# Optimization experiments

Measured on AMD Instinct MI355X. Metric: run time of the kernel, lower is better.

The kernel has to match this reference:

```python
import jax, jax.numpy as jnp
import numpy as np

D_IN, N_LAT, B, H, W = 512, 16384, 16, 16, 16

def setup_inputs() -> dict:
    key = jax.random.key(0)
    k1, k2, k3, k4, k5 = jax.random.split(key, 5)
    x = jax.random.normal(k1, (B, D_IN, H, W), dtype=jnp.float32)
    enc_w = jax.random.normal(k2, (N_LAT, D_IN), dtype=jnp.float32) / np.sqrt(D_IN)
    enc_b = jax.random.normal(k3, (N_LAT,), dtype=jnp.float32) * 0.01
    dec_w = jax.random.normal(k4, (D_IN, N_LAT), dtype=jnp.float32)
    # normalize_decoder=True: unit-norm columns (per latent)
    dec_w = dec_w / (jnp.linalg.norm(dec_w, axis=0, keepdims=True) + 1e-7)
    dec_b = jax.random.normal(k5, (D_IN,), dtype=jnp.float32) * 0.01
    return {"x": x, "enc_w": enc_w, "enc_b": enc_b, "dec_w": dec_w, "dec_b": dec_b, "k": 32}

def reference(x, enc_w, enc_b, dec_w, dec_b, k):
    # encoder: 1x1 conv == pointwise channel matmul, then ReLU
    pre = jax.nn.relu(jnp.einsum('bchw,lc->bhwl', x, enc_w) + enc_b)  # [B,H,W,L]
    # top-k over latent dim (last axis)
    top_acts, top_idx = jax.lax.top_k(pre, k)  # [B,H,W,k]
    # sparse decode: scatter-into-dense + 1x1 conv == gather decoder columns
    # and weighted sum (topk indices are distinct, so scatter == this gather-sum)
    w_g = dec_w.T[top_idx]                      # [B,H,W,k,d_in]
    sae_out = jnp.einsum('bhwk,bhwkd->bdhw', top_acts, w_g) + dec_b[None, :, None, None]
    e = sae_out - x
    l2_loss = jnp.sum(e.astype(jnp.float32) ** 2)
    mu = x.mean(axis=(0, 2, 3)).reshape(1, -1, 1, 1)
    total_variance = jnp.sum(((x - mu).astype(jnp.float32)) ** 2)
    fvu = (l2_loss / total_variance).astype(e.dtype)
    # match torch layout: [B, k, H, W]
    top_acts_out = jnp.transpose(top_acts, (0, 3, 1, 2))
    top_idx_out = jnp.transpose(top_idx, (0, 3, 1, 2))
    auxk_loss = jnp.zeros((), dtype=sae_out.dtype)
    multi_topk_fvu = jnp.zeros((), dtype=sae_out.dtype)
    return sae_out, top_acts_out, top_idx_out, fvu, auxk_loss, multi_topk_fvu
```

## Files before the change

### kernel.cpp

```cpp
#include <hip/hip_runtime.h>
#include <stdint.h>

typedef __attribute__((ext_vector_type(4))) int i32x4;

#define TN 2.45f
#define PMARG 0.10f
#define CAP 224
#define SORT2 128

__device__ inline float bf2f(unsigned short u) { return __uint_as_float(((unsigned int)u) << 16); }
__device__ inline unsigned short f2bf(float f) {
    unsigned int x = __float_as_uint(f);
    return (unsigned short)((x + 0x7FFFu + ((x >> 16) & 1u)) >> 16);
}

template <typename T>
__device__ inline void gload16(const T* g, T* l) {
    __builtin_amdgcn_global_load_lds((const __attribute__((address_space(1))) void*)g,
                                     (__attribute__((address_space(3))) void*)l, 16, 0, 0);
}

__global__ __launch_bounds__(256) void t1_x(const float* __restrict__ x, float* __restrict__ xTf,
                                            float* __restrict__ thrS,
                                            double* __restrict__ S, double* __restrict__ Q) {
    __shared__ float tile[64][65];
    int b = blockIdx.z, c0 = blockIdx.x * 64, hw0 = blockIdx.y * 64;
    int tid = threadIdx.x, g = tid >> 6, ln = tid & 63;
    for (int i = 0; i < 16; i++) {
        int cl = g * 16 + i;
        tile[cl][ln] = x[(size_t)(b * 512 + c0 + cl) * 256 + hw0 + ln];
    }
    __syncthreads();
    float s1 = 0.0f, s2 = 0.0f;
    for (int i = 0; i < 16; i++) {
        int hl = g * 16 + i;
        float v = tile[ln][hl];
        xTf[(size_t)(b * 256 + hw0 + hl) * 512 + c0 + ln] = v;
        s1 += v;
        s2 += v * v;
        float s = v * v;
        for (int off = 32; off; off >>= 1) s += __shfl_down(s, off, 64);
        if (ln == 0) atomicAdd(&thrS[b * 256 + hw0 + hl], s);
    }
    atomicAdd(&S[c0 + ln], (double)s1);
    atomicAdd(&Q[c0 + ln], (double)s2);
}

__device__ inline void quant_row(const float* __restrict__ src, signed char* __restrict__ dst,
                                 float* __restrict__ scale, int row, int lane) {
    const float4* s4 = (const float4*)(src + (size_t)row * 512);
    float4 a = s4[lane * 2], b = s4[lane * 2 + 1];
    float m = fmaxf(fmaxf(fmaxf(fabsf(a.x), fabsf(a.y)), fmaxf(fabsf(a.z), fabsf(a.w))),
                    fmaxf(fmaxf(fabsf(b.x), fabsf(b.y)), fmaxf(fabsf(b.z), fabsf(b.w))));
    for (int off = 32; off; off >>= 1) m = fmaxf(m, __shfl_xor(m, off, 64));
    m = fmaxf(m, 1e-20f);
    float inv = 127.0f / m;
    int q0 = __float2int_rn(a.x * inv), q1 = __float2int_rn(a.y * inv);
    int q2 = __float2int_rn(a.z * inv), q3 = __float2int_rn(a.w * inv);
    int q4 = __float2int_rn(b.x * inv), q5 = __float2int_rn(b.y * inv);
    int q6 = __float2int_rn(b.z * inv), q7 = __float2int_rn(b.w * inv);
    unsigned int w0 = (q0 & 255) | ((q1 & 255) << 8) | ((q2 & 255) << 16) | ((unsigned)(q3 & 255) << 24);
    unsigned int w1 = (q4 & 255) | ((q5 & 255) << 8) | ((q6 & 255) << 16) | ((unsigned)(q7 & 255) << 24);
    *(uint2*)(dst + (size_t)row * 512 + lane * 8) = make_uint2(w0, w1);
    if (lane == 0) scale[row] = m * (1.0f / 127.0f);
}

__global__ __launch_bounds__(256) void k_quant(const float* __restrict__ xTf, signed char* __restrict__ xq,
                                               float* __restrict__ sx, const float* __restrict__ enc_w,
                                               signed char* __restrict__ wq, float* __restrict__ sw) {
    int r = blockIdx.x * 4 + (threadIdx.x >> 6), lane = threadIdx.x & 63;
    if (r < 4096) quant_row(xTf, xq, sx, r, lane);
    else quant_row(enc_w, wq, sw, r - 4096, lane);
}

__global__ __launch_bounds__(256) void t3_decw(const float* __restrict__ w, unsigned short* __restrict__ wT) {
    __shared__ float tile[64][65];
    int l0 = blockIdx.x * 64, d0 = blockIdx.y * 64;
    int tid = threadIdx.x, g = tid >> 6, ln = tid & 63;
    for (int i = 0; i < 16; i++) {
        int dl = g * 16 + i;
        tile[dl][ln] = w[(size_t)(d0 + dl) * 16384 + l0 + ln];
    }
    __syncthreads();
    for (int i = 0; i < 16; i++) {
        int ll = g * 16 + i;
        wT[(size_t)(l0 + ll) * 512 + d0 + ln] = f2bf(tile[ln][ll]);
    }
}

#define SBAR                                   \
    __builtin_amdgcn_sched_barrier(0);         \
    __builtin_amdgcn_s_barrier();              \
    __builtin_amdgcn_sched_barrier(0);
#define VMW4 { asm volatile("s_waitcnt vmcnt(4)" ::: "memory"); __builtin_amdgcn_sched_barrier(0); }
#define VMW0 { asm volatile("s_waitcnt vmcnt(0)" ::: "memory"); __builtin_amdgcn_sched_barrier(0); }

__global__ __launch_bounds__(256) void k_gemm(const signed char* __restrict__ xq,
                                              const signed char* __restrict__ wq,
                                              const float* __restrict__ sx, const float* __restrict__ sw,
                                              const float* __restrict__ thrS,
                                              int* __restrict__ cnt, unsigned int* __restrict__ cand) {
    __shared__ __align__(16) signed char As[3][128 * 64];
    __shared__ __align__(16) signed char Bs[3][128 * 64];
    int tid = threadIdx.x, wid = tid >> 6, lane = tid & 63;

    int lin = blockIdx.x + blockIdx.y * gridDim.x;
    int swz = (lin & 7) * 512 + (lin >> 3);
    int bx = swz >> 5;
    int by = swz & 31;
    int m0 = by * 128, n0 = bx * 128;
    int wr = wid >> 1, wc = wid & 1;

    i32x4 acc[4][4];
#pragma unroll
    for (int mi = 0; mi < 4; mi++)
#pragma unroll
        for (int ni = 0; ni < 4; ni++)
#pragma unroll
            for (int j = 0; j < 4; j++) acc[mi][ni][j] = 0;

    int srow = lane >> 2;

#define STAGE(bufi, kt)                                                                            \
    {                                                                                              \
        signed char* Ad = &As[bufi][0];                                                            \
        signed char* Bd = &Bs[bufi][0];                                                            \
        _Pragma("unroll")                                                                          \
        for (int i_ = 0; i_ < 2; i_++) {                                                           \
            int ch_ = wid * 2 + i_;                                                                \
            int row_ = ch_ * 16 + srow;                                                            \
            int sc_ = (((lane & 3) ^ ((row_ >> 1) & 3)) << 4);                                     \
            gload16(xq + (size_t)(m0 + row_) * 512 + (kt) + sc_, Ad + ch_ * 1024);                 \
            gload16(wq + (size_t)(n0 + row_) * 512 + (kt) + sc_, Bd + ch_ * 1024);                 \
        }                                                                                          \
    }

    STAGE(0, 0)
    STAGE(1, 64)
#pragma unroll
    for (int t = 0; t < 8; t++) {
        int cur = t % 3;
        if (t < 7) VMW4
        else VMW0
        SBAR
        if (t < 6) STAGE((t + 2) % 3, (t + 2) * 64)
        const signed char* Ac = &As[cur][0];
        const signed char* Bc = &Bs[cur][0];
        i32x4 a[4], b[4];
#pragma unroll
        for (int mi = 0; mi < 4; mi++) {
            int r = wr * 64 + mi * 16 + (lane & 15);
            int slot = (lane >> 4) ^ ((r >> 1) & 3);
            a[mi] = *(const i32x4*)&Ac[r * 64 + slot * 16];
        }
#pragma unroll
        for (int ni = 0; ni < 4; ni++) {
            int r = wc * 64 + ni * 16 + (lane & 15);
            int slot = (lane >> 4) ^ ((r >> 1) & 3);
            b[ni] = *(const i32x4*)&Bc[r * 64 + slot * 16];
        }
#pragma unroll
        for (int mi = 0; mi < 4; mi++)
#pragma unroll
            for (int ni = 0; ni < 4; ni++)
                acc[mi][ni] = __builtin_amdgcn_mfma_i32_16x16x64_i8(a[mi], b[ni], acc[mi][ni], 0, 0, 0);
    }
#undef STAGE

    float swl[4];
#pragma unroll
    for (int ni = 0; ni < 4; ni++) swl[ni] = sw[n0 + wc * 64 + ni * 16 + (lane & 15)];
#pragma unroll
    for (int mi = 0; mi < 4; mi++)
#pragma unroll
        for (int j = 0; j < 4; j++) {
            int pixel = m0 + wr * 64 + mi * 16 + (lane >> 4) * 4 + j;
            float tv = TN * sqrtf(thrS[pixel] * (1.0f / 512.0f));
            float sxp = sx[pixel];
#pragma unroll
            for (int ni = 0; ni < 4; ni++) {
                float v = (float)acc[mi][ni][j] * (sxp * swl[ni]);
                if (v >= tv) {
                    int lat = n0 + wc * 64 + ni * 16 + (lane & 15);
                    int slot = atomicAdd(&cnt[pixel], 1);
                    if (slot < CAP) cand[pixel * CAP + slot] = ((unsigned)f2bf(v) << 16) | (unsigned)lat;
                }
            }
        }
}

__global__ __launch_bounds__(256) void k_topk(const float* __restrict__ xTf, const float* __restrict__ enc_w,
                                              const float* __restrict__ enc_b, const int* __restrict__ cnt,
                                              const unsigned int* __restrict__ cand,
                                              const unsigned short* __restrict__ dwT,
                                              const float* __restrict__ dec_b,
                                              float* __restrict__ out_acts, float* __restrict__ out_idx,
                                              float* __restrict__ out_sae, double* __restrict__ l2acc) {
    __shared__ __align__(16) float xrow[512];
    __shared__ unsigned long long skey2[SORT2];
    __shared__ int npool;
    __shared__ float sa[32];
    __shared__ int si[32];
    __shared__ double red[256];
    int p = blockIdx.x, tid = threadIdx.x;
    for (int i = tid; i < 512; i += 256) xrow[i] = xTf[(size_t)p * 512 + i];
    if (tid < SORT2) skey2[tid] = ~0ull;
    if (tid == 0) npool = 0;
    int c = cnt[p];
    if (c > CAP) c = CAP;
    unsigned int pk = (tid < c) ? cand[p * CAP + tid] : 0u;
    unsigned int bfb = pk >> 16;
    int lo = 0, hi = 65535;
    for (int it = 0; it < 16; it++) {
        int mid = (lo + hi + 1) >> 1;
        int n = __syncthreads_count(tid < c && bfb >= (unsigned)mid);
        if (n >= 32) lo = mid; else hi = mid - 1;
    }
    float pthr = bf2f((unsigned short)lo) - PMARG;
    __syncthreads();
    if (tid < c && bf2f((unsigned short)bfb) >= pthr) {
        int slot = atomicAdd(&npool, 1);
        if (slot < SORT2) {
            int lat = (int)(pk & 16383u);
            const float4* w4 = (const float4*)(enc_w + (size_t)lat * 512);
            const float4* x4 = (const float4*)xrow;
            float acc = 0.0f;
            for (int q = 0; q < 128; q++) {
                float4 w = w4[q];
                float4 xv = x4[q];
                acc = __fmaf_rn(xv.x, w.x, acc);
                acc = __fmaf_rn(xv.y, w.y, acc);
                acc = __fmaf_rn(xv.z, w.z, acc);
                acc = __fmaf_rn(xv.w, w.w, acc);
            }
            float pre = __fadd_rn(acc, enc_b[lat]);
            unsigned long long key;
            if (pre > 0.0f) {
                key = ((unsigned long long)(0xFFFFFFFFu - __float_as_uint(pre)) << 32) | (unsigned)lat;
            } else {
                key = 0xFFFFFFFF00000000ull | (unsigned)lat;
            }
            skey2[slot] = key;
        }
    }
    __syncthreads();
    for (int ks = 2; ks <= SORT2; ks <<= 1) {
        for (int jj = ks >> 1; jj > 0; jj >>= 1) {
            int i = tid;
            if (i < SORT2) {
                int ixj = i ^ jj;
                if (ixj > i) {
                    bool up = ((i & ks) == 0);
                    unsigned long long a = skey2[i], b2 = skey2[ixj];
                    if (up ? (a > b2) : (a < b2)) { skey2[i] = b2; skey2[ixj] = a; }
                }
            }
            __syncthreads();
        }
    }
    int b = p >> 8, hw = p & 255;
    if (tid < 32) {
        unsigned long long key = skey2[tid];
        unsigned int fb = 0xFFFFFFFFu - (unsigned int)(key >> 32);
        float act = fmaxf(__uint_as_float(fb), 0.0f);
        int lat = (int)(key & 16383u);
        sa[tid] = act;
        si[tid] = lat;
        out_acts[(size_t)b * 8192 + tid * 256 + hw] = act;
        out_idx[(size_t)b * 8192 + tid * 256 + hw] = (float)lat;
    }
    __syncthreads();
    float a0 = dec_b[tid], a1 = dec_b[tid + 256];
    for (int j = 0; j < 32; j++) {
        float a = sa[j];
        const unsigned short* r = dwT + (size_t)si[j] * 512;
        a0 += a * bf2f(r[tid]);
        a1 += a * bf2f(r[tid + 256]);
    }
    size_t o0 = (size_t)b * 131072 + (size_t)tid * 256 + hw;
    size_t o1 = o0 + 65536;
    out_sae[o0] = a0;
    out_sae[o1] = a1;
    float e0 = a0 - xrow[tid], e1 = a1 - xrow[tid + 256];
    red[tid] = (double)e0 * e0 + (double)e1 * e1;
    __syncthreads();
    for (int s = 128; s; s >>= 1) {
        if (tid < s) red[tid] += red[tid + s];
        __syncthreads();
    }
    if (tid == 0) atomicAdd(l2acc, red[0]);
}

__global__ __launch_bounds__(256) void k_fin(const double* __restrict__ l2, const double* __restrict__ S,
                                             const double* __restrict__ Q, float* __restrict__ out_sc) {
    __shared__ double red[256];
    int tid = threadIdx.x;
    double tv = 0;
    for (int c = tid; c < 512; c += 256) tv += Q[c] - S[c] * S[c] * (1.0 / 4096.0);
    red[tid] = tv;
    __syncthreads();
    for (int s = 128; s; s >>= 1) {
        if (tid < s) red[tid] += red[tid + s];
        __syncthreads();
    }
    if (tid == 0) {
        double fvu = l2[0] / red[0];
        out_sc[0] = (float)fvu;
        out_sc[1] = 0.0f;
        out_sc[2] = 0.0f;
    }
}

extern "C" void kernel_launch(void* const* d_in, const int* in_sizes, int n_in,
                              void* d_out, int out_size, void* d_ws, size_t ws_size,
                              hipStream_t stream) {
    const float* x = (const float*)d_in[0];
    const float* enc_w = (const float*)d_in[1];
    const float* enc_b = (const float*)d_in[2];
    const float* dec_w = (const float*)d_in[3];
    const float* dec_b = (const float*)d_in[4];
    (void)in_sizes; (void)n_in; (void)out_size; (void)ws_size;

    char* ws = (char*)d_ws;
    float* xTf = (float*)ws;
    signed char* xq = (signed char*)(ws + 8388608);
    signed char* wq = (signed char*)(ws + 10485760);
    unsigned short* dwT = (unsigned short*)(ws + 18874368);
    unsigned int* cand = (unsigned int*)(ws + 35651584);
    int* cnt = (int*)(ws + 39321600);
    float* thrS = (float*)(ws + 39337984);
    double* S = (double*)(ws + 39354368);
    double* Q = (double*)(ws + 39358464);
    double* l2 = (double*)(ws + 39362560);
    float* sx = (float*)(ws + 39366656);
    float* sw = (float*)(ws + 39383040);

    float* out = (float*)d_out;
    float* out_sae = out;
    float* out_acts = out + 2097152;
    float* out_idx = out + 2228224;
    float* out_sc = out + 2359296;

    hipMemsetAsync(cnt, 0, 16384 + 16384 + 4096 + 4096 + 8, stream);

    t1_x<<<dim3(8, 4, 16), 256, 0, stream>>>(x, xTf, thrS, S, Q);
    k_quant<<<5120, 256, 0, stream>>>(xTf, xq, sx, enc_w, wq, sw);
    t3_decw<<<dim3(256, 8), 256, 0, stream>>>(dec_w, dwT);
    k_gemm<<<dim3(128, 32), 256, 0, stream>>>(xq, wq, sx, sw, thrS, cnt, cand);
    k_topk<<<4096, 256, 0, stream>>>(xTf, enc_w, enc_b, cnt, cand, dwT, dec_b,
                                     out_acts, out_idx, out_sae, l2);
    k_fin<<<1, 256, 0, stream>>>(l2, S, Q, out_sc);
}
```

Baseline: 285.5 us.

## Load GEMM operands directly from global into registers, dropping LDS staging

The int8 encoder GEMM no longer stages A and B tiles through a triple-buffered LDS pipeline with barriers. Each wave now loads its MFMA fragments straight from global memory into registers and double-buffers them in registers across the K loop. This removes LDS traffic and the workgroup barriers. In exchange, the two waves that share a row or column tile each fetch it separately, doubling global/L2 reads, and register pressure goes up.

```diff
diff --git a/kernel.cpp b/kernel.cpp
--- a/kernel.cpp
+++ b/kernel.cpp
@@ -12,12 +12,6 @@
 __device__ inline unsigned short f2bf(float f) {
     unsigned int x = __float_as_uint(f);
     return (unsigned short)((x + 0x7FFFu + ((x >> 16) & 1u)) >> 16);
-}
-
-template <typename T>
-__device__ inline void gload16(const T* g, T* l) {
-    __builtin_amdgcn_global_load_lds((const __attribute__((address_space(1))) void*)g,
-                                     (__attribute__((address_space(3))) void*)l, 16, 0, 0);
 }
 
 __global__ __launch_bounds__(256) void t1_x(const float* __restrict__ x, float* __restrict__ xTf,
@@ -88,20 +82,11 @@
     }
 }
 
-#define SBAR                                   \
-    __builtin_amdgcn_sched_barrier(0);         \
-    __builtin_amdgcn_s_barrier();              \
-    __builtin_amdgcn_sched_barrier(0);
-#define VMW4 { asm volatile("s_waitcnt vmcnt(4)" ::: "memory"); __builtin_amdgcn_sched_barrier(0); }
-#define VMW0 { asm volatile("s_waitcnt vmcnt(0)" ::: "memory"); __builtin_amdgcn_sched_barrier(0); }
-
 __global__ __launch_bounds__(256) void k_gemm(const signed char* __restrict__ xq,
                                               const signed char* __restrict__ wq,
                                               const float* __restrict__ sx, const float* __restrict__ sw,
                                               const float* __restrict__ thrS,
                                               int* __restrict__ cnt, unsigned int* __restrict__ cand) {
-    __shared__ __align__(16) signed char As[3][128 * 64];
-    __shared__ __align__(16) signed char Bs[3][128 * 64];
     int tid = threadIdx.x, wid = tid >> 6, lane = tid & 63;
 
     int lin = blockIdx.x + blockIdx.y * gridDim.x;
@@ -111,6 +96,9 @@
     int m0 = by * 128, n0 = bx * 128;
     int wr = wid >> 1, wc = wid & 1;
 
+    const signed char* Abase = xq + (size_t)(m0 + wr * 64 + (lane & 15)) * 512 + ((lane >> 4) << 4);
+    const signed char* Bbase = wq + (size_t)(n0 + wc * 64 + (lane & 15)) * 512 + ((lane >> 4) << 4);
+
     i32x4 acc[4][4];
 #pragma unroll
     for (int mi = 0; mi < 4; mi++)
@@ -119,53 +107,29 @@
 #pragma unroll
             for (int j = 0; j < 4; j++) acc[mi][ni][j] = 0;
 
-    int srow = lane >> 2;
-
-#define STAGE(bufi, kt)                                                                            \
-    {                                                                                              \
-        signed char* Ad = &As[bufi][0];                                                            \
-        signed char* Bd = &Bs[bufi][0];                                                            \
-        _Pragma("unroll")                                                                          \
-        for (int i_ = 0; i_ < 2; i_++) {                                                           \
-            int ch_ = wid * 2 + i_;                                                                \
-            int row_ = ch_ * 16 + srow;                                                            \
-            int sc_ = (((lane & 3) ^ ((row_ >> 1) & 3)) << 4);                                     \
-            gload16(xq + (size_t)(m0 + row_) * 512 + (kt) + sc_, Ad + ch_ * 1024);                 \
-            gload16(wq + (size_t)(n0 + row_) * 512 + (kt) + sc_, Bd + ch_ * 1024);                 \
-        }                                                                                          \
-    }
-
-    STAGE(0, 0)
-    STAGE(1, 64)
+    i32x4 a[2][4], b[2][4];
+#pragma unroll
+    for (int mi = 0; mi < 4; mi++) {
+        a[0][mi] = *(const i32x4*)(Abase + (size_t)(mi * 16) * 512);
+        b[0][mi] = *(const i32x4*)(Bbase + (size_t)(mi * 16) * 512);
+    }
 #pragma unroll
     for (int t = 0; t < 8; t++) {
-        int cur = t % 3;
-        if (t < 7) VMW4
-        else VMW0
-        SBAR
-        if (t < 6) STAGE((t + 2) % 3, (t + 2) * 64)
-        const signed char* Ac = &As[cur][0];
-        const signed char* Bc = &Bs[cur][0];
-        i32x4 a[4], b[4];
-#pragma unroll
-        for (int mi = 0; mi < 4; mi++) {
-            int r = wr * 64 + mi * 16 + (lane & 15);
-            int slot = (lane >> 4) ^ ((r >> 1) & 3);
-            a[mi] = *(const i32x4*)&Ac[r * 64 + slot * 16];
+        int cur = t & 1;
+        if (t < 7) {
+            int kt = (t + 1) * 64;
+#pragma unroll
+            for (int mi = 0; mi < 4; mi++) {
+                a[cur ^ 1][mi] = *(const i32x4*)(Abase + (size_t)(mi * 16) * 512 + kt);
+                b[cur ^ 1][mi] = *(const i32x4*)(Bbase + (size_t)(mi * 16) * 512 + kt);
+            }
         }
 #pragma unroll
-        for (int ni = 0; ni < 4; ni++) {
-            int r = wc * 64 + ni * 16 + (lane & 15);
-            int slot = (lane >> 4) ^ ((r >> 1) & 3);
-            b[ni] = *(const i32x4*)&Bc[r * 64 + slot * 16];
-        }
-#pragma unroll
         for (int mi = 0; mi < 4; mi++)
 #pragma unroll
             for (int ni = 0; ni < 4; ni++)
-                acc[mi][ni] = __builtin_amdgcn_mfma_i32_16x16x64_i8(a[mi], b[ni], acc[mi][ni], 0, 0, 0);
-    }
-#undef STAGE
+                acc[mi][ni] = __builtin_amdgcn_mfma_i32_16x16x64_i8(a[cur][mi], b[cur][ni], acc[mi][ni], 0, 0, 0);
+    }
 
     float swl[4];
 #pragma unroll
```

Result: slower. 359.9 us (+26.1%).
